# Kernel optimization log

Measured on AMD Instinct MI355X. Metric: run time of the kernel, lower is better.

Reference implementation:

```python
import jax, jax.numpy as jnp
import numpy as np

B, T, H = 2, 1024, 4096
HK, HV, DK, DV = 8, 32, 64, 64
VPK = HV // HK            # value heads per key head = 4
KEY_DIM = HK * DK         # 512
VAL_DIM = HV * DV         # 2048
CONV_DIM = 2 * KEY_DIM + VAL_DIM  # 3072
KSZ = 4
EPS = 1e-5
L2_EPS = 1e-6


def _l2norm(x):
    return x * jax.lax.rsqrt(jnp.sum(x * x, axis=-1, keepdims=True) + L2_EPS)


def setup_inputs() -> dict:
    key = jax.random.key(0)
    ks = jax.random.split(key, 8)
    s = 0.02
    return {
        "hidden_states": jax.random.normal(ks[0], (B, T, H), jnp.float32),
        "W_qkvz": jax.random.normal(ks[1], (H, 2 * KEY_DIM + 2 * VAL_DIM), jnp.float32) * s,
        "W_ba": jax.random.normal(ks[2], (H, 2 * HV), jnp.float32) * s,
        "conv_w": jax.random.normal(ks[3], (CONV_DIM, KSZ), jnp.float32) * 0.1,
        "dt_bias": jnp.ones((HV,), jnp.float32),
        "A_log": jnp.log(jax.random.uniform(ks[4], (HV,), jnp.float32, 1.0, 16.0)),
        "norm_w": jnp.ones((DV,), jnp.float32),
        "W_out": jax.random.normal(ks[5], (VAL_DIM, H), jnp.float32) * s,
    }


def _forward(hidden_states, W_qkvz, W_ba, conv_w, dt_bias, A_log, norm_w, W_out):
    # --- projections ---
    qkvz = hidden_states @ W_qkvz                       # [B,T,5120]
    ba = hidden_states @ W_ba                           # [B,T,64]
    # fix_query_key_value_ordering: per key head [q(Dk), k(Dk), v(vpk*Dv), z(vpk*Dv)]
    qkvz = qkvz.reshape(B, T, HK, 2 * DK + 2 * VPK * DV)
    q = qkvz[..., :DK]                                  # [B,T,HK,DK]
    k = qkvz[..., DK:2 * DK]
    v = qkvz[..., 2 * DK:2 * DK + VPK * DV].reshape(B, T, HV, DV)
    z = qkvz[..., 2 * DK + VPK * DV:].reshape(B, T, HV, DV)
    ba = ba.reshape(B, T, HK, 2 * VPK)
    b = ba[..., :VPK].reshape(B, T, HV)
    a = ba[..., VPK:].reshape(B, T, HV)

    # --- causal depthwise conv over concatenated qkv, then silu ---
    mixed = jnp.concatenate(
        [q.reshape(B, T, KEY_DIM), k.reshape(B, T, KEY_DIM), v.reshape(B, T, VAL_DIM)], axis=-1)
    padded = jnp.pad(mixed, ((0, 0), (KSZ - 1, 0), (0, 0)))
    conv = sum(padded[:, j:j + T, :] * conv_w[:, j] for j in range(KSZ))
    conv = jax.nn.silu(conv)
    q = conv[..., :KEY_DIM].reshape(B, T, HK, DK)
    k = conv[..., KEY_DIM:2 * KEY_DIM].reshape(B, T, HK, DK)
    v = conv[..., 2 * KEY_DIM:].reshape(B, T, HV, DV)

    # --- fused GDN gating: g = -exp(A_log)*softplus(a+dt_bias), beta = sigmoid(b) ---
    g = -jnp.exp(A_log) * jax.nn.softplus(a + dt_bias)  # [B,T,HV]
    beta = jax.nn.sigmoid(b)                            # [B,T,HV]

    # --- q/k l2 norm + scale, broadcast key heads to value heads ---
    q = _l2norm(q) * (DK ** -0.5)
    k = _l2norm(k)
    q = jnp.repeat(q, VPK, axis=2)                      # [B,T,HV,DK]
    k = jnp.repeat(k, VPK, axis=2)

    # --- gated delta-rule recurrence over time ---
    def step(S, inp):
        qt, kt, vt, gt, bt = inp                        # qt/kt [B,HV,DK], vt [B,HV,DV]
        S = S * jnp.exp(gt)[..., None, None]            # decay
        pred = jnp.einsum('bhk,bhkv->bhv', kt, S)
        delta = (vt - pred) * bt[..., None]
        S = S + jnp.einsum('bhk,bhv->bhkv', kt, delta)
        o = jnp.einsum('bhk,bhkv->bhv', qt, S)
        return S, o

    xs = (q.transpose(1, 0, 2, 3), k.transpose(1, 0, 2, 3), v.transpose(1, 0, 2, 3),
          g.transpose(1, 0, 2), beta.transpose(1, 0, 2))
    S0 = jnp.zeros((B, HV, DK, DV), q.dtype)
    _, o = jax.lax.scan(step, S0, xs)                   # [T,B,HV,DV]
    o = o.transpose(1, 0, 2, 3)                         # [B,T,HV,DV]

    # --- gated RMSNorm (norm before gate) + out projection ---
    o_n = o * jax.lax.rsqrt(jnp.mean(o * o, axis=-1, keepdims=True) + EPS) * norm_w
    o_n = o_n * jax.nn.silu(z)
    return o_n.reshape(B, T, VAL_DIM) @ W_out           # [B,T,H]


def reference(hidden_states, W_qkvz, W_ba, conv_w, dt_bias, A_log, norm_w, W_out):
    return _forward(hidden_states, W_qkvz, W_ba, conv_w, dt_bias, A_log, norm_w, W_out)
```

## Files before the change

### kernel.cpp

```cpp
#include <hip/hip_runtime.h>
#include <hip/hip_bf16.h>
#include <cstdint>
#include <cstddef>


typedef __attribute__((ext_vector_type(8))) short short8;
typedef __attribute__((ext_vector_type(4))) float f32x4;

__device__ __forceinline__ short f2bf(float f) {
  union { float f; unsigned u; } x; x.f = f;
  unsigned r = x.u + 0x7fffu + ((x.u >> 16) & 1u);
  return (short)(r >> 16);
}

__device__ __forceinline__ void gl_lds16(const short* g, short* l) {
  __builtin_amdgcn_global_load_lds(
      (const __attribute__((address_space(1))) void*)g,
      (__attribute__((address_space(3))) void*)l, 16, 0, 0);
}

__global__ __launch_bounds__(256) void to_bf16_kernel(const float* __restrict__ x,
                                                      short* __restrict__ y) {
  int i = blockIdx.x * 256 + threadIdx.x;
  float4 v = ((const float4*)x)[i];
  ushort4 r;
  r.x = (unsigned short)f2bf(v.x);
  r.y = (unsigned short)f2bf(v.y);
  r.z = (unsigned short)f2bf(v.z);
  r.w = (unsigned short)f2bf(v.w);
  ((ushort4*)y)[i] = r;
}

__global__ __launch_bounds__(256) void transpose_w1(const float* __restrict__ Wq,
                                                    const float* __restrict__ Wba,
                                                    short* __restrict__ Wt) {
  __shared__ float tile[32][33];
  int n0 = blockIdx.x * 32;
  int k0 = blockIdx.y * 32;
  int t = threadIdx.x;
  int r = t >> 5;
  int c = t & 31;
#pragma unroll
  for (int i = 0; i < 4; ++i) {
    int kl = r + i * 8;
    int n = n0 + c;
    float v = 0.f;
    if (n < 5120) v = Wq[(size_t)(k0 + kl) * 5120 + n];
    else if (n < 5184) v = Wba[(size_t)(k0 + kl) * 64 + (n - 5120)];
    tile[kl][c] = v;
  }
  __syncthreads();
#pragma unroll
  for (int i = 0; i < 4; ++i) {
    int nl = r + i * 8;
    int kl = c;
    Wt[(size_t)(n0 + nl) * 4096 + k0 + kl] = f2bf(tile[kl][nl]);
  }
}

__global__ __launch_bounds__(256) void transpose_w2(const float* __restrict__ W,
                                                    short* __restrict__ Wt) {
  __shared__ float tile[32][33];
  int n0 = blockIdx.x * 32;
  int k0 = blockIdx.y * 32;
  int t = threadIdx.x;
  int r = t >> 5;
  int c = t & 31;
#pragma unroll
  for (int i = 0; i < 4; ++i) {
    int kl = r + i * 8;
    tile[kl][c] = W[(size_t)(k0 + kl) * 4096 + n0 + c];
  }
  __syncthreads();
#pragma unroll
  for (int i = 0; i < 4; ++i) {
    int nl = r + i * 8;
    int kl = c;
    Wt[(size_t)(n0 + nl) * 2048 + k0 + kl] = f2bf(tile[kl][nl]);
  }
}

template <bool GUARD_N>
__global__ __launch_bounds__(128) void gemm128w2(const short* __restrict__ A,
                                                 const short* __restrict__ Bt,
                                                 float* __restrict__ C,
                                                 int N, int K, int MT) {
  __shared__ __align__(16) short As[3 * 4096];
  __shared__ __align__(16) short Bs[3 * 4096];
  const int tid = threadIdx.x;
  const int w = tid >> 6, lane = tid & 63;

  const int nwg = gridDim.x;
  const int bid = blockIdx.x;
  const int swz = (bid & 7) * (nwg >> 3) + (bid >> 3);
  const int m0 = (swz % MT) * 128;
  const int n0 = (swz / MT) * 128;

  const int rp0 = tid >> 3, q0 = tid & 7;
  const int mm0 = q0 ^ (rp0 & 7);
  const int srow = rp0 * 2 + (mm0 >> 2);
  const int scol = (mm0 & 3) << 3;
  const short* Ag = A + (size_t)(m0 + srow) * K + scol;
  const short* Bg = Bt + (size_t)(n0 + srow) * K + scol;
  const size_t rstep = (size_t)32 * K;

  const int fr = lane & 15;
  const int s = lane >> 4;
  int aoff[4], boff[8];
#pragma unroll
  for (int i = 0; i < 4; ++i) {
    int row = w * 64 + i * 16 + fr;
    int rp = row >> 1;
    int q = (((row & 1) << 2) | s) ^ (rp & 7);
    aoff[i] = (rp * 8 + q) * 8;
  }
#pragma unroll
  for (int j = 0; j < 8; ++j) {
    int row = j * 16 + fr;
    int rp = row >> 1;
    int q = (((row & 1) << 2) | s) ^ (rp & 7);
    boff[j] = (rp * 8 + q) * 8;
  }

  f32x4 acc[4][8];
#pragma unroll
  for (int i = 0; i < 4; ++i)
#pragma unroll
    for (int j = 0; j < 8; ++j) acc[i][j] = (f32x4){0.f, 0.f, 0.f, 0.f};

  const int NKT = K >> 5;

#define STAGE_A(kt, bb)                                                  \
  { const short* g = Ag + (size_t)(kt) * 32;                             \
    gl_lds16(g,             &As[(bb) * 4096 + (w << 9)]);                \
    gl_lds16(g + rstep,     &As[(bb) * 4096 + 1024 + (w << 9)]);         \
    gl_lds16(g + 2 * rstep, &As[(bb) * 4096 + 2048 + (w << 9)]);         \
    gl_lds16(g + 3 * rstep, &As[(bb) * 4096 + 3072 + (w << 9)]); }
#define STAGE_B(kt, bb)                                                  \
  { const short* g = Bg + (size_t)(kt) * 32;                             \
    gl_lds16(g,             &Bs[(bb) * 4096 + (w << 9)]);                \
    gl_lds16(g + rstep,     &Bs[(bb) * 4096 + 1024 + (w << 9)]);         \
    gl_lds16(g + 2 * rstep, &Bs[(bb) * 4096 + 2048 + (w << 9)]);         \
    gl_lds16(g + 3 * rstep, &Bs[(bb) * 4096 + 3072 + (w << 9)]); }

  STAGE_A(0, 0); STAGE_B(0, 0);
  STAGE_A(1, 1); STAGE_B(1, 1);
  asm volatile("s_waitcnt vmcnt(8)" ::: "memory");
  __builtin_amdgcn_s_barrier();
  __builtin_amdgcn_sched_barrier(0);

  int bi = 0;
  for (int kt = 0; kt < NKT; ++kt) {
    int bi2 = bi - 1; if (bi2 < 0) bi2 = 2;
    const short* Ab = &As[bi * 4096];
    const short* Bb = &Bs[bi * 4096];
    short8 af[4], bf[4];
#pragma unroll
    for (int i = 0; i < 4; ++i) af[i] = *(const short8*)&Ab[aoff[i]];
#pragma unroll
    for (int j = 0; j < 4; ++j) bf[j] = *(const short8*)&Bb[boff[j]];
    if (kt + 2 < NKT) STAGE_A(kt + 2, bi2);
    __builtin_amdgcn_s_barrier();
    asm volatile("s_waitcnt lgkmcnt(0)" ::: "memory");
    __builtin_amdgcn_sched_barrier(0);
    __builtin_amdgcn_s_setprio(1);
#pragma unroll
    for (int i = 0; i < 4; ++i)
#pragma unroll
      for (int j = 0; j < 4; ++j)
        acc[i][j] = __builtin_amdgcn_mfma_f32_16x16x32_bf16(af[i], bf[j], acc[i][j], 0, 0, 0);
    __builtin_amdgcn_s_setprio(0);
    __builtin_amdgcn_sched_barrier(0);
#pragma unroll
    for (int j = 0; j < 4; ++j) bf[j] = *(const short8*)&Bb[boff[j + 4]];
    if (kt + 2 < NKT) STAGE_B(kt + 2, bi2);
    if (kt < NKT - 2) { asm volatile("s_waitcnt vmcnt(8)" ::: "memory"); }
    else              { asm volatile("s_waitcnt vmcnt(0)" ::: "memory"); }
    __builtin_amdgcn_s_barrier();
    asm volatile("s_waitcnt lgkmcnt(0)" ::: "memory");
    __builtin_amdgcn_sched_barrier(0);
    __builtin_amdgcn_s_setprio(1);
#pragma unroll
    for (int i = 0; i < 4; ++i)
#pragma unroll
      for (int j = 0; j < 4; ++j)
        acc[i][j + 4] = __builtin_amdgcn_mfma_f32_16x16x32_bf16(af[i], bf[j], acc[i][j + 4], 0, 0, 0);
    __builtin_amdgcn_s_setprio(0);
    __builtin_amdgcn_sched_barrier(0);
    __builtin_amdgcn_s_barrier();
    ++bi; if (bi == 3) bi = 0;
  }
#undef STAGE_A
#undef STAGE_B

  const int rbase = (lane >> 4) << 2;
#pragma unroll
  for (int i = 0; i < 4; ++i) {
#pragma unroll
    for (int j = 0; j < 8; ++j) {
      int col = n0 + j * 16 + fr;
      if (GUARD_N && col >= N) continue;
      int row = m0 + w * 64 + i * 16 + rbase;
#pragma unroll
      for (int r = 0; r < 4; ++r)
        C[(size_t)(row + r) * N + col] = acc[i][j][r];
    }
  }
}

__global__ __launch_bounds__(256) void conv_kernel(const float* __restrict__ qkvz,
                                                   const float* __restrict__ conv_w,
                                                   float* __restrict__ mix) {
  __shared__ float sq[1024];
  __shared__ float scale[16];
  int bt = blockIdx.x;
  int t = bt & 1023;
  int tid = threadIdx.x;
  for (int c = tid; c < 3072; c += 256) {
    int col;
    if (c < 512) {
      col = (c >> 6) * 640 + (c & 63);
    } else if (c < 1024) {
      int c2 = c - 512;
      col = (c2 >> 6) * 640 + 64 + (c2 & 63);
    } else {
      int c3 = c - 1024;
      int hv = c3 >> 6;
      col = (hv >> 2) * 640 + 128 + (hv & 3) * 64 + (c3 & 63);
    }
    float acc = 0.f;
#pragma unroll
    for (int j = 0; j < 4; ++j) {
      int tt = t - 3 + j;
      if (tt >= 0) acc += qkvz[(size_t)(bt - 3 + j) * 5184 + col] * conv_w[c * 4 + j];
    }
    float sv = acc / (1.f + __expf(-acc));
    if (c < 1024)
      sq[c] = sv;
    else
      mix[(size_t)bt * 3072 + c] = sv;
  }
  __syncthreads();
  int g = tid >> 4, l = tid & 15;
  float p = 0.f;
#pragma unroll
  for (int i = 0; i < 4; ++i) {
    float v = sq[g * 64 + l * 4 + i];
    p += v * v;
  }
  p += __shfl_xor(p, 1);
  p += __shfl_xor(p, 2);
  p += __shfl_xor(p, 4);
  p += __shfl_xor(p, 8);
  if (l == 0) scale[g] = rsqrtf(p + 1e-6f);
  __syncthreads();
  for (int c = tid; c < 1024; c += 256) {
    float s = scale[c >> 6] * ((c < 512) ? 0.125f : 1.f);
    mix[(size_t)bt * 3072 + c] = sq[c] * s;
  }
}

__global__ __launch_bounds__(256) void gate_kernel(const float* __restrict__ qkvz,
                                                   const float* __restrict__ dt_bias,
                                                   const float* __restrict__ A_log,
                                                   float* __restrict__ gb,
                                                   float* __restrict__ beta) {
  int i = blockIdx.x * 256 + threadIdx.x;
  int hv = i & 31;
  int bt = i >> 5;
  int hk = hv >> 2, vp = hv & 3;
  const float* row = qkvz + (size_t)bt * 5184 + 5120 + hk * 8;
  float bv = row[vp];
  float av = row[4 + vp];
  float x = av + dt_bias[hv];
  float sp = (x > 20.f) ? x : log1pf(expf(x));
  gb[i] = -expf(A_log[hv]) * sp;
  beta[i] = 1.f / (1.f + expf(-bv));
}

__global__ __launch_bounds__(256) void precompute_kernel(
    const float* __restrict__ mix, const float* __restrict__ gbuf,
    const float* __restrict__ betab, float* __restrict__ Wbuf,
    float* __restrict__ Pbuf, float* __restrict__ Rbuf, float* __restrict__ cbuf) {
  __shared__ float Kt[64][68];
  __shared__ float Vb[64][68];
  __shared__ float AM[64][68];
  __shared__ float Mm[64][68];
  __shared__ float Tb[16][17];
  __shared__ float cs[64], bb[64];

  const int u = blockIdx.x;
  const int chunk = u & 15, hv = (u >> 4) & 31, b = u >> 9;
  const int hk = hv >> 2;
  const int t0g = b * 1024 + chunk * 64;
  const int tid = threadIdx.x;
  const int tr = tid >> 2, q4 = tid & 3;

  {
    const float* mrow = mix + (size_t)(t0g + tr) * 3072;
#pragma unroll
    for (int e = 0; e < 4; ++e) {
      int c0 = q4 * 16 + e * 4;
      float4 kv = *(const float4*)(mrow + 512 + hk * 64 + c0);
      Kt[c0 + 0][tr] = kv.x; Kt[c0 + 1][tr] = kv.y;
      Kt[c0 + 2][tr] = kv.z; Kt[c0 + 3][tr] = kv.w;
      *(float4*)&Vb[tr][c0] = *(const float4*)(mrow + 1024 + hv * 64 + c0);
    }
  }
  if (tid < 64) {
    cs[tid] = gbuf[(size_t)(t0g + tid) * 32 + hv];
    bb[tid] = betab[(size_t)(t0g + tid) * 32 + hv];
  }
  __syncthreads();
  for (int off = 1; off < 64; off <<= 1) {
    float v = 0.f;
    if (tid < 64 && tid >= off) v = cs[tid - off];
    __syncthreads();
    if (tid < 64) cs[tid] += v;
    __syncthreads();
  }
  if (tid < 64) cbuf[(size_t)u * 64 + tid] = cs[tid];

  {
    float acc[16];
#pragma unroll
    for (int i = 0; i < 16; ++i) acc[i] = 0.f;
    for (int d = 0; d < 64; ++d) {
      float kv = Kt[d][tr];
#pragma unroll
      for (int e = 0; e < 4; ++e) {
        float4 ks = *(const float4*)&Kt[d][q4 * 16 + e * 4];
        acc[e * 4 + 0] += kv * ks.x; acc[e * 4 + 1] += kv * ks.y;
        acc[e * 4 + 2] += kv * ks.z; acc[e * 4 + 3] += kv * ks.w;
      }
    }
    float bt_ = bb[tr], ct_ = cs[tr];
#pragma unroll
    for (int j = 0; j < 16; ++j) {
      int s = q4 * 16 + j;
      AM[tr][s] = (s < tr) ? bt_ * acc[j] * __expf(ct_ - cs[s]) : 0.f;
    }
  }
  __syncthreads();

  for (int i = tid; i < 64 * 68; i += 256) (&Mm[0][0])[i] = 0.f;
  __syncthreads();
  if (tid < 64) {
    int blk = tid >> 4, j = tid & 15, base = blk * 16;
    Mm[base][base + j] = (j == 0) ? 1.f : 0.f;
    for (int r = 1; r < 16; ++r) {
      float sum = 0.f;
      for (int s = 0; s < r; ++s) sum += AM[base + r][base + s] * Mm[base + s][base + j];
      Mm[base + r][base + j] = ((r == j) ? 1.f : 0.f) - sum;
    }
  }
  __syncthreads();
  for (int d = 1; d < 4; ++d) {
    for (int j = 0; j + d < 4; ++j) {
      int i = j + d;
      int r = tid >> 4, c = tid & 15;
      float tsum = 0.f;
      for (int kb = j; kb < i; ++kb)
        for (int uu = 0; uu < 16; ++uu)
          tsum += AM[i * 16 + r][kb * 16 + uu] * Mm[kb * 16 + uu][j * 16 + c];
      Tb[r][c] = tsum;
      __syncthreads();
      float msum = 0.f;
      for (int uu = 0; uu < 16; ++uu)
        msum += Mm[i * 16 + r][i * 16 + uu] * Tb[uu][c];
      __syncthreads();
      Mm[i * 16 + r][j * 16 + c] = -msum;
      __syncthreads();
    }
  }

  {
    const float* mrow = mix + (size_t)(t0g + tr) * 3072 + hk * 64;
#pragma unroll
    for (int e = 0; e < 4; ++e) {
      int c0 = q4 * 16 + e * 4;
      float4 qv = *(const float4*)(mrow + c0);
      AM[c0 + 0][tr] = qv.x; AM[c0 + 1][tr] = qv.y;
      AM[c0 + 2][tr] = qv.z; AM[c0 + 3][tr] = qv.w;
    }
  }
  __syncthreads();

  {
    float acc[16];
#pragma unroll
    for (int i = 0; i < 16; ++i) acc[i] = 0.f;
    for (int d = 0; d < 64; ++d) {
      float qv = AM[d][tr];
#pragma unroll
      for (int e = 0; e < 4; ++e) {
        float4 ks = *(const float4*)&Kt[d][q4 * 16 + e * 4];
        acc[e * 4 + 0] += qv * ks.x; acc[e * 4 + 1] += qv * ks.y;
        acc[e * 4 + 2] += qv * ks.z; acc[e * 4 + 3] += qv * ks.w;
      }
    }
    float ct_ = cs[tr];
#pragma unroll
    for (int e = 0; e < 4; ++e) {
      int s0 = q4 * 16 + e * 4;
      float4 pv;
      pv.x = (s0 + 0 <= tr) ? acc[e * 4 + 0] * __expf(ct_ - cs[s0 + 0]) : 0.f;
      pv.y = (s0 + 1 <= tr) ? acc[e * 4 + 1] * __expf(ct_ - cs[s0 + 1]) : 0.f;
      pv.z = (s0 + 2 <= tr) ? acc[e * 4 + 2] * __expf(ct_ - cs[s0 + 2]) : 0.f;
      pv.w = (s0 + 3 <= tr) ? acc[e * 4 + 3] * __expf(ct_ - cs[s0 + 3]) : 0.f;
      *(float4*)&Pbuf[(size_t)u * 4096 + tr * 64 + s0] = pv;
    }
  }
  __syncthreads();

  {
    float vals[16];
#pragma unroll
    for (int j = 0; j < 16; ++j) vals[j] = Kt[q4 * 16 + j][tr];
    float sc = bb[tr] * __expf(cs[tr]);
    __syncthreads();
#pragma unroll
    for (int j = 0; j < 16; ++j) Kt[tr][q4 * 16 + j] = vals[j] * sc;
  }
  __syncthreads();

  {
    float acc[16];
#pragma unroll
    for (int i = 0; i < 16; ++i) acc[i] = 0.f;
    for (int s = 0; s < 64; ++s) {
      float m = Mm[tr][s];
#pragma unroll
      for (int e = 0; e < 4; ++e) {
        float4 kk = *(const float4*)&Kt[s][q4 * 16 + e * 4];
        acc[e * 4 + 0] += m * kk.x; acc[e * 4 + 1] += m * kk.y;
        acc[e * 4 + 2] += m * kk.z; acc[e * 4 + 3] += m * kk.w;
      }
    }
#pragma unroll
    for (int e = 0; e < 4; ++e) {
      float4 wv = {acc[e * 4 + 0], acc[e * 4 + 1], acc[e * 4 + 2], acc[e * 4 + 3]};
      *(float4*)&Wbuf[(size_t)u * 4096 + tr * 64 + q4 * 16 + e * 4] = wv;
    }
  }
  {
    float acc[16];
#pragma unroll
    for (int i = 0; i < 16; ++i) acc[i] = 0.f;
    for (int s = 0; s < 64; ++s) {
      float m = Mm[tr][s] * bb[s];
#pragma unroll
      for (int e = 0; e < 4; ++e) {
        float4 vv = *(const float4*)&Vb[s][q4 * 16 + e * 4];
        acc[e * 4 + 0] += m * vv.x; acc[e * 4 + 1] += m * vv.y;
        acc[e * 4 + 2] += m * vv.z; acc[e * 4 + 3] += m * vv.w;
      }
    }
#pragma unroll
    for (int e = 0; e < 4; ++e) {
      float4 rv = {acc[e * 4 + 0], acc[e * 4 + 1], acc[e * 4 + 2], acc[e * 4 + 3]};
      *(float4*)&Rbuf[(size_t)u * 4096 + tr * 64 + q4 * 16 + e * 4] = rv;
    }
  }
}

__global__ __launch_bounds__(256) void precompute2_kernel(
    const float* __restrict__ mix, const float* __restrict__ cbuf,
    float* __restrict__ Wbuf, float* __restrict__ Pbuf, float* __restrict__ Rbuf,
    float* __restrict__ Hbuf) {
  __shared__ float At[64][132];
  __shared__ float Bsm[64][188];

  const int u = blockIdx.x;
  const int chunk = u & 15, hv = (u >> 4) & 31, b = u >> 9;
  const int hk = hv >> 2;
  const int t0g = b * 1024 + chunk * 64;
  const int tid = threadIdx.x;
  const int tr = tid >> 2, q4 = tid & 3;

  const float c63 = cbuf[(size_t)u * 64 + 63];
  const float csr = cbuf[(size_t)u * 64 + tr];
  const float sKv = __expf(c63 - csr);

  {
    const float* Pr = Pbuf + (size_t)u * 4096 + tr * 64;
#pragma unroll
    for (int e = 0; e < 4; ++e) {
      int k0 = q4 * 16 + e * 4;
      float4 p4 = *(const float4*)(Pr + k0);
      At[k0 + 0][tr] = p4.x; At[k0 + 1][tr] = p4.y;
      At[k0 + 2][tr] = p4.z; At[k0 + 3][tr] = p4.w;
    }
    const float* Kr = mix + (size_t)(t0g + tr) * 3072 + 512 + hk * 64;
#pragma unroll
    for (int e = 0; e < 4; ++e) {
      int n = q4 * 16 + e * 4;
      float4 k4 = *(const float4*)(Kr + n);
      float4 o4 = {k4.x * sKv, k4.y * sKv, k4.z * sKv, k4.w * sKv};
      *(float4*)&At[tr][64 + n] = o4;
    }
  }
  {
    const float* Wr = Wbuf + (size_t)u * 4096 + tr * 64;
    const float* Rr = Rbuf + (size_t)u * 4096 + tr * 64;
#pragma unroll
    for (int e = 0; e < 4; ++e) {
      int n = q4 * 16 + e * 4;
      int cp = n + ((n >> 3) << 2);
      *(float4*)&Bsm[tr][cp] = *(const float4*)(Wr + n);
      *(float4*)&Bsm[tr][cp + 96] = *(const float4*)(Rr + n);
    }
  }
  __syncthreads();

  const int m0 = (tid >> 4) << 3;
  const int n0 = (tid & 15) << 3;
  const int cb = n0 + ((n0 >> 3) << 2);
  float acc[8][8];
#pragma unroll
  for (int i = 0; i < 8; ++i)
#pragma unroll
    for (int j = 0; j < 8; ++j) acc[i][j] = 0.f;

  for (int k = 0; k < 64; ++k) {
    float4 a0 = *(const float4*)&At[k][m0];
    float4 a1 = *(const float4*)&At[k][m0 + 4];
    float4 b0 = *(const float4*)&Bsm[k][cb];
    float4 b1 = *(const float4*)&Bsm[k][cb + 4];
    float am[8] = {a0.x, a0.y, a0.z, a0.w, a1.x, a1.y, a1.z, a1.w};
    float bn[8] = {b0.x, b0.y, b0.z, b0.w, b1.x, b1.y, b1.z, b1.w};
#pragma unroll
    for (int i = 0; i < 8; ++i)
#pragma unroll
      for (int j = 0; j < 8; ++j) acc[i][j] += am[i] * bn[j];
  }

  if (m0 < 64) {
    if (n0 < 64) {
#pragma unroll
      for (int i = 0; i < 8; ++i) {
        int t = m0 + i;
        float ee = __expf(cbuf[(size_t)u * 64 + t]);
        const float* Qr = mix + (size_t)(t0g + t) * 3072 + hk * 64 + n0;
        float4 q0 = *(const float4*)(Qr);
        float4 q1 = *(const float4*)(Qr + 4);
        float4 g0 = {q0.x * ee - acc[i][0], q0.y * ee - acc[i][1],
                     q0.z * ee - acc[i][2], q0.w * ee - acc[i][3]};
        float4 g1 = {q1.x * ee - acc[i][4], q1.y * ee - acc[i][5],
                     q1.z * ee - acc[i][6], q1.w * ee - acc[i][7]};
        float* dst = Wbuf + (size_t)u * 4096 + t * 64 + n0;
        *(float4*)dst = g0; *(float4*)(dst + 4) = g1;
      }
    } else {
#pragma unroll
      for (int i = 0; i < 8; ++i) {
        float* dst = Rbuf + (size_t)u * 4096 + (m0 + i) * 64 + (n0 - 64);
        float4 r0 = {acc[i][0], acc[i][1], acc[i][2], acc[i][3]};
        float4 r1 = {acc[i][4], acc[i][5], acc[i][6], acc[i][7]};
        *(float4*)dst = r0; *(float4*)(dst + 4) = r1;
      }
    }
  } else {
    if (n0 < 64) {
#pragma unroll
      for (int i = 0; i < 8; ++i) {
        float* dst = Hbuf + (size_t)u * 4096 + (m0 - 64 + i) * 64 + n0;
        float4 h0 = {acc[i][0], acc[i][1], acc[i][2], acc[i][3]};
        float4 h1 = {acc[i][4], acc[i][5], acc[i][6], acc[i][7]};
        *(float4*)dst = h0; *(float4*)(dst + 4) = h1;
      }
    } else {
#pragma unroll
      for (int i = 0; i < 8; ++i) {
        float* dst = Pbuf + (size_t)u * 4096 + (m0 - 64 + i) * 64 + (n0 - 64);
        float4 k0v = {acc[i][0], acc[i][1], acc[i][2], acc[i][3]};
        float4 k1v = {acc[i][4], acc[i][5], acc[i][6], acc[i][7]};
        *(float4*)dst = k0v; *(float4*)(dst + 4) = k1v;
      }
    }
  }
}

__global__ __launch_bounds__(512) void chunk_scan_kernel(
    const float* __restrict__ Gbuf, const float* __restrict__ Hbuf,
    const float* __restrict__ ORbuf, const float* __restrict__ KRbuf,
    const float* __restrict__ cbuf, float* __restrict__ o) {
  __shared__ float Gs[64][68], Hs[64][68];
  __shared__ float St[16][68];

  const int bid = blockIdx.x;
  const int vs = bid & 3, hv = (bid >> 2) & 31, b = bid >> 7;
  const int bh = b * 32 + hv;
  const int ubase = bh * 16;
  const int tid = threadIdx.x;
  const int tr = tid >> 3, q8 = tid & 7;
  const int c0 = q8 * 2, c1 = q8 * 2 + 1;

  for (int i = tid; i < 16 * 68; i += 512) (&St[0][0])[i] = 0.f;

  float4 GN[2], HN[2];
  float2 ORn, KRn;
  float e63n = 0.f;

#define ISSUE(ch)                                                               \
  {                                                                             \
    size_t uu = (size_t)(ubase + (ch));                                         \
    _Pragma("unroll") for (int i = 0; i < 2; ++i) {                             \
      GN[i] = ((const float4*)(Gbuf + uu * 4096))[tid + 512 * i];               \
      HN[i] = ((const float4*)(Hbuf + uu * 4096))[tid + 512 * i];               \
    }                                                                           \
    ORn = *(const float2*)(ORbuf + uu * 4096 + tr * 64 + vs * 16 + q8 * 2);     \
    KRn = *(const float2*)(KRbuf + uu * 4096 + tr * 64 + vs * 16 + q8 * 2);     \
    e63n = cbuf[uu * 64 + 63];                                                  \
  }

#define COMMIT()                                                                \
  {                                                                             \
    _Pragma("unroll") for (int i = 0; i < 2; ++i) {                             \
      int flat = (tid + 512 * i) * 4;                                           \
      int rr = flat >> 6, cc = flat & 63;                                       \
      *(float4*)&Gs[rr][cc] = GN[i];                                            \
      *(float4*)&Hs[rr][cc] = HN[i];                                            \
    }                                                                           \
  }

  ISSUE(0);
  COMMIT();
  float2 ORv = ORn, KRv = KRn;
  float e63 = __expf(e63n);
  __syncthreads();

  for (int c = 0; c < 16; ++c) {
    if (c < 15) ISSUE(c + 1);
    float op0 = ORv.x, op1 = ORv.y, sn0 = KRv.x, sn1 = KRv.y;
    float sold0 = St[c0][tr], sold1 = St[c1][tr];
#pragma unroll
    for (int i = 0; i < 16; ++i) {
      float4 g4 = *(const float4*)&Gs[tr][i * 4];
      float4 h4 = *(const float4*)&Hs[tr][i * 4];
      float4 sa = *(const float4*)&St[c0][i * 4];
      float4 sb = *(const float4*)&St[c1][i * 4];
      op0 += g4.x * sa.x + g4.y * sa.y + g4.z * sa.z + g4.w * sa.w;
      op1 += g4.x * sb.x + g4.y * sb.y + g4.z * sb.z + g4.w * sb.w;
      sn0 -= h4.x * sa.x + h4.y * sa.y + h4.z * sa.z + h4.w * sa.w;
      sn1 -= h4.x * sb.x + h4.y * sb.y + h4.z * sb.z + h4.w * sb.w;
    }
    *(float2*)&o[((size_t)(bh * 4 + vs) * 1024 + c * 64 + tr) * 16 + q8 * 2] =
        (float2){op0, op1};
    float snew0 = sold0 * e63 + sn0;
    float snew1 = sold1 * e63 + sn1;
    __syncthreads();
    St[c0][tr] = snew0;
    St[c1][tr] = snew1;
    if (c < 15) {
      COMMIT();
      ORv = ORn; KRv = KRn; e63 = __expf(e63n);
    }
    __syncthreads();
  }
#undef ISSUE
#undef COMMIT
}

__global__ __launch_bounds__(256) void rms_gate_kernel(const float* __restrict__ o,
                                                       const float* __restrict__ qkvz,
                                                       const float* __restrict__ norm_w,
                                                       short* __restrict__ on) {
  int bid = blockIdx.x;
  int bh = bid >> 8;
  int tg = bid & 255;
  int b = bh >> 5, hv = bh & 31;
  int t = tg * 4 + (threadIdx.x >> 6);
  int d = threadIdx.x & 63;
  int bt = b * 1024 + t;
  int hk = hv >> 2, vp = hv & 3;
  float x = o[((size_t)(bh * 4 + (d >> 4)) * 1024 + t) * 16 + (d & 15)];
  float ss = x * x;
  ss += __shfl_xor(ss, 1);
  ss += __shfl_xor(ss, 2);
  ss += __shfl_xor(ss, 4);
  ss += __shfl_xor(ss, 8);
  ss += __shfl_xor(ss, 16);
  ss += __shfl_xor(ss, 32);
  float sc = rsqrtf(ss * (1.f / 64.f) + 1e-5f);
  float z = qkvz[(size_t)bt * 5184 + hk * 640 + 384 + vp * 64 + d];
  float val = x * sc * norm_w[d] * (z / (1.f + __expf(-z)));
  on[((size_t)bt * 32 + hv) * 64 + d] = f2bf(val);
}

extern "C" void kernel_launch(void* const* d_in, const int* in_sizes, int n_in,
                              void* d_out, int out_size, void* d_ws, size_t ws_size,
                              hipStream_t stream) {
  const float* hidden = (const float*)d_in[0];
  const float* W_qkvz = (const float*)d_in[1];
  const float* W_ba = (const float*)d_in[2];
  const float* conv_w = (const float*)d_in[3];
  const float* dt_bias = (const float*)d_in[4];
  const float* A_log = (const float*)d_in[5];
  const float* norm_w = (const float*)d_in[6];
  const float* W_out = (const float*)d_in[7];
  float* out = (float*)d_out;

  char* ws = (char*)d_ws;
  short* A_bf = (short*)(ws + 0);
  float* Hbuf = (float*)(ws + 0);
  short* Wt1 = (short*)(ws + 16777216);
  short* Wt2 = (short*)(ws + 59768832);
  float* qkvz = (float*)(ws + 76546048);
  float* mix = (float*)(ws + 119013376);
  float* gbuf = (float*)(ws + 144179200);
  float* beta = (float*)(ws + 144441344);
  float* o = (float*)(ws + 144703488);
  short* on = (short*)(ws + 161480704);
  float* Wbuf = (float*)(ws + 169869312);
  float* Pbuf = (float*)(ws + 186646528);
  float* Rbuf = (float*)(ws + 203423744);
  float* cbuf = (float*)(ws + 220200960);

  to_bf16_kernel<<<8192, 256, 0, stream>>>(hidden, A_bf);
  transpose_w1<<<dim3(164, 128), 256, 0, stream>>>(W_qkvz, W_ba, Wt1);
  transpose_w2<<<dim3(128, 64), 256, 0, stream>>>(W_out, Wt2);
  gemm128w2<true><<<656, 128, 0, stream>>>(A_bf, Wt1, qkvz, 5184, 4096, 16);
  conv_kernel<<<2048, 256, 0, stream>>>(qkvz, conv_w, mix);
  gate_kernel<<<256, 256, 0, stream>>>(qkvz, dt_bias, A_log, gbuf, beta);
  precompute_kernel<<<1024, 256, 0, stream>>>(mix, gbuf, beta, Wbuf, Pbuf, Rbuf, cbuf);
  precompute2_kernel<<<1024, 256, 0, stream>>>(mix, cbuf, Wbuf, Pbuf, Rbuf, Hbuf);
  chunk_scan_kernel<<<256, 512, 0, stream>>>(Wbuf, Hbuf, Rbuf, Pbuf, cbuf, o);
  rms_gate_kernel<<<16384, 256, 0, stream>>>(o, qkvz, norm_w, on);
  gemm128w2<false><<<512, 128, 0, stream>>>(on, Wt2, out, 4096, 2048, 16);
}
```

Measured before the change: 556.9 us.

## Use 4-wave GEMM, fuse gate into conv, register-tile precompute matmuls

The bf16 GEMM now runs 256 threads in a 2x2 wave grid, each wave computing a 64x64 sub-tile instead of 64x128, which lowers per-wave accumulator registers and adds waves per block. The separate gate kernel is folded into the conv kernel, saving one launch. The small 64x64 matmuls in precompute_kernel are rewritten with 4x4 register blocking, and the W and R products are fused into one loop so Mm is read only once. The change raises occupancy and reuse, at the cost of more barrier participants per block and different LDS access patterns.

Measured after the change: 536.0 us. 1.04x faster.

```diff
diff --git a/kernel.cpp b/kernel.cpp
--- a/kernel.cpp
+++ b/kernel.cpp
@@ -81,14 +81,15 @@
 }
 
 template <bool GUARD_N>
-__global__ __launch_bounds__(128) void gemm128w2(const short* __restrict__ A,
-                                                 const short* __restrict__ Bt,
-                                                 float* __restrict__ C,
-                                                 int N, int K, int MT) {
+__global__ __launch_bounds__(256) void gemm128p(const short* __restrict__ A,
+                                                const short* __restrict__ Bt,
+                                                float* __restrict__ C,
+                                                int N, int K, int MT) {
   __shared__ __align__(16) short As[3 * 4096];
   __shared__ __align__(16) short Bs[3 * 4096];
   const int tid = threadIdx.x;
   const int w = tid >> 6, lane = tid & 63;
+  const int wm = w >> 1, wn = w & 1;
 
   const int nwg = gridDim.x;
   const int bid = blockIdx.x;
@@ -96,56 +97,53 @@
   const int m0 = (swz % MT) * 128;
   const int n0 = (swz / MT) * 128;
 
-  const int rp0 = tid >> 3, q0 = tid & 7;
+  const int p0 = w * 64 + lane;
+  const int rp0 = p0 >> 3, q0 = p0 & 7;
   const int mm0 = q0 ^ (rp0 & 7);
   const int srow = rp0 * 2 + (mm0 >> 2);
   const int scol = (mm0 & 3) << 3;
   const short* Ag = A + (size_t)(m0 + srow) * K + scol;
   const short* Bg = Bt + (size_t)(n0 + srow) * K + scol;
-  const size_t rstep = (size_t)32 * K;
+  const size_t rstep = (size_t)64 * K;
 
   const int fr = lane & 15;
   const int s = lane >> 4;
-  int aoff[4], boff[8];
+  int aoff[4], boff[4];
 #pragma unroll
   for (int i = 0; i < 4; ++i) {
-    int row = w * 64 + i * 16 + fr;
+    int row = wm * 64 + i * 16 + fr;
     int rp = row >> 1;
     int q = (((row & 1) << 2) | s) ^ (rp & 7);
     aoff[i] = (rp * 8 + q) * 8;
   }
 #pragma unroll
-  for (int j = 0; j < 8; ++j) {
-    int row = j * 16 + fr;
+  for (int j = 0; j < 4; ++j) {
+    int row = wn * 64 + j * 16 + fr;
     int rp = row >> 1;
     int q = (((row & 1) << 2) | s) ^ (rp & 7);
     boff[j] = (rp * 8 + q) * 8;
   }
 
-  f32x4 acc[4][8];
+  f32x4 acc[4][4];
 #pragma unroll
   for (int i = 0; i < 4; ++i)
 #pragma unroll
-    for (int j = 0; j < 8; ++j) acc[i][j] = (f32x4){0.f, 0.f, 0.f, 0.f};
+    for (int j = 0; j < 4; ++j) acc[i][j] = (f32x4){0.f, 0.f, 0.f, 0.f};
 
   const int NKT = K >> 5;
 
-#define STAGE_A(kt, bb)                                                  \
-  { const short* g = Ag + (size_t)(kt) * 32;                             \
-    gl_lds16(g,             &As[(bb) * 4096 + (w << 9)]);                \
-    gl_lds16(g + rstep,     &As[(bb) * 4096 + 1024 + (w << 9)]);         \
-    gl_lds16(g + 2 * rstep, &As[(bb) * 4096 + 2048 + (w << 9)]);         \
-    gl_lds16(g + 3 * rstep, &As[(bb) * 4096 + 3072 + (w << 9)]); }
-#define STAGE_B(kt, bb)                                                  \
-  { const short* g = Bg + (size_t)(kt) * 32;                             \
-    gl_lds16(g,             &Bs[(bb) * 4096 + (w << 9)]);                \
-    gl_lds16(g + rstep,     &Bs[(bb) * 4096 + 1024 + (w << 9)]);         \
-    gl_lds16(g + 2 * rstep, &Bs[(bb) * 4096 + 2048 + (w << 9)]);         \
-    gl_lds16(g + 3 * rstep, &Bs[(bb) * 4096 + 3072 + (w << 9)]); }
+#define STAGE_A(kt, bb)                                                \
+  { const short* g = Ag + (size_t)(kt) * 32;                           \
+    gl_lds16(g,         &As[(bb) * 4096 + w * 512]);                   \
+    gl_lds16(g + rstep, &As[(bb) * 4096 + 2048 + w * 512]); }
+#define STAGE_B(kt, bb)                                                \
+  { const short* g = Bg + (size_t)(kt) * 32;                           \
+    gl_lds16(g,         &Bs[(bb) * 4096 + w * 512]);                   \
+    gl_lds16(g + rstep, &Bs[(bb) * 4096 + 2048 + w * 512]); }
 
   STAGE_A(0, 0); STAGE_B(0, 0);
   STAGE_A(1, 1); STAGE_B(1, 1);
-  asm volatile("s_waitcnt vmcnt(8)" ::: "memory");
+  asm volatile("s_waitcnt vmcnt(4)" ::: "memory");
   __builtin_amdgcn_s_barrier();
   __builtin_amdgcn_sched_barrier(0);
 
@@ -154,9 +152,9 @@
     int bi2 = bi - 1; if (bi2 < 0) bi2 = 2;
     const short* Ab = &As[bi * 4096];
     const short* Bb = &Bs[bi * 4096];
-    short8 af[4], bf[4];
-#pragma unroll
-    for (int i = 0; i < 4; ++i) af[i] = *(const short8*)&Ab[aoff[i]];
+    short8 af[2], bf[4];
+#pragma unroll
+    for (int i = 0; i < 2; ++i) af[i] = *(const short8*)&Ab[aoff[i]];
 #pragma unroll
     for (int j = 0; j < 4; ++j) bf[j] = *(const short8*)&Bb[boff[j]];
     if (kt + 2 < NKT) STAGE_A(kt + 2, bi2);
@@ -165,26 +163,26 @@
     __builtin_amdgcn_sched_barrier(0);
     __builtin_amdgcn_s_setprio(1);
 #pragma unroll
-    for (int i = 0; i < 4; ++i)
+    for (int i = 0; i < 2; ++i)
 #pragma unroll
       for (int j = 0; j < 4; ++j)
         acc[i][j] = __builtin_amdgcn_mfma_f32_16x16x32_bf16(af[i], bf[j], acc[i][j], 0, 0, 0);
     __builtin_amdgcn_s_setprio(0);
     __builtin_amdgcn_sched_barrier(0);
 #pragma unroll
-    for (int j = 0; j < 4; ++j) bf[j] = *(const short8*)&Bb[boff[j + 4]];
+    for (int i = 0; i < 2; ++i) af[i] = *(const short8*)&Ab[aoff[i + 2]];
     if (kt + 2 < NKT) STAGE_B(kt + 2, bi2);
-    if (kt < NKT - 2) { asm volatile("s_waitcnt vmcnt(8)" ::: "memory"); }
+    if (kt < NKT - 2) { asm volatile("s_waitcnt vmcnt(4)" ::: "memory"); }
     else              { asm volatile("s_waitcnt vmcnt(0)" ::: "memory"); }
     __builtin_amdgcn_s_barrier();
     asm volatile("s_waitcnt lgkmcnt(0)" ::: "memory");
     __builtin_amdgcn_sched_barrier(0);
     __builtin_amdgcn_s_setprio(1);
 #pragma unroll
-    for (int i = 0; i < 4; ++i)
+    for (int i = 0; i < 2; ++i)
 #pragma unroll
       for (int j = 0; j < 4; ++j)
-        acc[i][j + 4] = __builtin_amdgcn_mfma_f32_16x16x32_bf16(af[i], bf[j], acc[i][j + 4], 0, 0, 0);
+        acc[i + 2][j] = __builtin_amdgcn_mfma_f32_16x16x32_bf16(af[i], bf[j], acc[i + 2][j], 0, 0, 0);
     __builtin_amdgcn_s_setprio(0);
     __builtin_amdgcn_sched_barrier(0);
     __builtin_amdgcn_s_barrier();
@@ -197,10 +195,10 @@
 #pragma unroll
   for (int i = 0; i < 4; ++i) {
 #pragma unroll
-    for (int j = 0; j < 8; ++j) {
-      int col = n0 + j * 16 + fr;
+    for (int j = 0; j < 4; ++j) {
+      int col = n0 + wn * 64 + j * 16 + fr;
       if (GUARD_N && col >= N) continue;
-      int row = m0 + w * 64 + i * 16 + rbase;
+      int row = m0 + wm * 64 + i * 16 + rbase;
 #pragma unroll
       for (int r = 0; r < 4; ++r)
         C[(size_t)(row + r) * N + col] = acc[i][j][r];
@@ -210,7 +208,11 @@
 
 __global__ __launch_bounds__(256) void conv_kernel(const float* __restrict__ qkvz,
                                                    const float* __restrict__ conv_w,
-                                                   float* __restrict__ mix) {
+                                                   const float* __restrict__ dt_bias,
+                                                   const float* __restrict__ A_log,
+                                                   float* __restrict__ mix,
+                                                   float* __restrict__ gb,
+                                                   float* __restrict__ beta) {
   __shared__ float sq[1024];
   __shared__ float scale[16];
   int bt = blockIdx.x;
@@ -240,6 +242,17 @@
     else
       mix[(size_t)bt * 3072 + c] = sv;
   }
+  if (tid < 32) {
+    int hv2 = tid;
+    int hk2 = hv2 >> 2, vp = hv2 & 3;
+    const float* row = qkvz + (size_t)bt * 5184 + 5120 + hk2 * 8;
+    float bv = row[vp];
+    float av = row[4 + vp];
+    float x = av + dt_bias[hv2];
+    float sp = (x > 20.f) ? x : log1pf(expf(x));
+    gb[(size_t)bt * 32 + hv2] = -expf(A_log[hv2]) * sp;
+    beta[(size_t)bt * 32 + hv2] = 1.f / (1.f + expf(-bv));
+  }
   __syncthreads();
   int g = tid >> 4, l = tid & 15;
   float p = 0.f;
@@ -258,24 +271,6 @@
     float s = scale[c >> 6] * ((c < 512) ? 0.125f : 1.f);
     mix[(size_t)bt * 3072 + c] = sq[c] * s;
   }
-}
-
-__global__ __launch_bounds__(256) void gate_kernel(const float* __restrict__ qkvz,
-                                                   const float* __restrict__ dt_bias,
-                                                   const float* __restrict__ A_log,
-                                                   float* __restrict__ gb,
-                                                   float* __restrict__ beta) {
-  int i = blockIdx.x * 256 + threadIdx.x;
-  int hv = i & 31;
-  int bt = i >> 5;
-  int hk = hv >> 2, vp = hv & 3;
-  const float* row = qkvz + (size_t)bt * 5184 + 5120 + hk * 8;
-  float bv = row[vp];
-  float av = row[4 + vp];
-  float x = av + dt_bias[hv];
-  float sp = (x > 20.f) ? x : log1pf(expf(x));
-  gb[i] = -expf(A_log[hv]) * sp;
-  beta[i] = 1.f / (1.f + expf(-bv));
 }
 
 __global__ __launch_bounds__(256) void precompute_kernel(
@@ -295,6 +290,7 @@
   const int t0g = b * 1024 + chunk * 64;
   const int tid = threadIdx.x;
   const int tr = tid >> 2, q4 = tid & 3;
+  const int r4 = tid >> 4, c4 = tid & 15;
 
   {
     const float* mrow = mix + (size_t)(t0g + tr) * 3072;
@@ -322,23 +318,35 @@
   if (tid < 64) cbuf[(size_t)u * 64 + tid] = cs[tid];
 
   {
-    float acc[16];
-#pragma unroll
-    for (int i = 0; i < 16; ++i) acc[i] = 0.f;
+    float acc[4][4];
+#pragma unroll
+    for (int i = 0; i < 4; ++i)
+#pragma unroll
+      for (int j = 0; j < 4; ++j) acc[i][j] = 0.f;
     for (int d = 0; d < 64; ++d) {
-      float kv = Kt[d][tr];
-#pragma unroll
-      for (int e = 0; e < 4; ++e) {
-        float4 ks = *(const float4*)&Kt[d][q4 * 16 + e * 4];
-        acc[e * 4 + 0] += kv * ks.x; acc[e * 4 + 1] += kv * ks.y;
-        acc[e * 4 + 2] += kv * ks.z; acc[e * 4 + 3] += kv * ks.w;
+      float4 a4 = *(const float4*)&Kt[d][r4 * 4];
+      float4 b4 = *(const float4*)&Kt[d][c4 * 4];
+      float av[4] = {a4.x, a4.y, a4.z, a4.w};
+      float bv[4] = {b4.x, b4.y, b4.z, b4.w};
+#pragma unroll
+      for (int i = 0; i < 4; ++i)
+#pragma unroll
+        for (int j = 0; j < 4; ++j) acc[i][j] += av[i] * bv[j];
+    }
+    float4 cc = *(const float4*)&cs[c4 * 4];
+    float ccv[4] = {cc.x, cc.y, cc.z, cc.w};
+#pragma unroll
+    for (int i = 0; i < 4; ++i) {
+      int row = r4 * 4 + i;
+      float bt_ = bb[row], ct_ = cs[row];
+      float ov[4];
+#pragma unroll
+      for (int j = 0; j < 4; ++j) {
+        int sc = c4 * 4 + j;
+        ov[j] = (sc < row) ? bt_ * acc[i][j] * __expf(ct_ - ccv[j]) : 0.f;
       }
-    }
-    float bt_ = bb[tr], ct_ = cs[tr];
-#pragma unroll
-    for (int j = 0; j < 16; ++j) {
-      int s = q4 * 16 + j;
-      AM[tr][s] = (s < tr) ? bt_ * acc[j] * __expf(ct_ - cs[s]) : 0.f;
+      float4 o4 = {ov[0], ov[1], ov[2], ov[3]};
+      *(float4*)&AM[row][c4 * 4] = o4;
     }
   }
   __syncthreads();
@@ -387,28 +395,35 @@
   __syncthreads();
 
   {
-    float acc[16];
-#pragma unroll
-    for (int i = 0; i < 16; ++i) acc[i] = 0.f;
+    float acc[4][4];
+#pragma unroll
+    for (int i = 0; i < 4; ++i)
+#pragma unroll
+      for (int j = 0; j < 4; ++j) acc[i][j] = 0.f;
     for (int d = 0; d < 64; ++d) {
-      float qv = AM[d][tr];
-#pragma unroll
-      for (int e = 0; e < 4; ++e) {
-        float4 ks = *(const float4*)&Kt[d][q4 * 16 + e * 4];
-        acc[e * 4 + 0] += qv * ks.x; acc[e * 4 + 1] += qv * ks.y;
-        acc[e * 4 + 2] += qv * ks.z; acc[e * 4 + 3] += qv * ks.w;
+      float4 a4 = *(const float4*)&AM[d][r4 * 4];
+      float4 b4 = *(const float4*)&Kt[d][c4 * 4];
+      float av[4] = {a4.x, a4.y, a4.z, a4.w};
+      float bv[4] = {b4.x, b4.y, b4.z, b4.w};
+#pragma unroll
+      for (int i = 0; i < 4; ++i)
+#pragma unroll
+        for (int j = 0; j < 4; ++j) acc[i][j] += av[i] * bv[j];
+    }
+    float4 cc = *(const float4*)&cs[c4 * 4];
+    float ccv[4] = {cc.x, cc.y, cc.z, cc.w};
+#pragma unroll
+    for (int i = 0; i < 4; ++i) {
+      int row = r4 * 4 + i;
+      float ct_ = cs[row];
+      float pv[4];
+#pragma unroll
+      for (int j = 0; j < 4; ++j) {
+        int sc = c4 * 4 + j;
+        pv[j] = (sc <= row) ? acc[i][j] * __expf(ct_ - ccv[j]) : 0.f;
       }
-    }
-    float ct_ = cs[tr];
-#pragma unroll
-    for (int e = 0; e < 4; ++e) {
-      int s0 = q4 * 16 + e * 4;
-      float4 pv;
-      pv.x = (s0 + 0 <= tr) ? acc[e * 4 + 0] * __expf(ct_ - cs[s0 + 0]) : 0.f;
-      pv.y = (s0 + 1 <= tr) ? acc[e * 4 + 1] * __expf(ct_ - cs[s0 + 1]) : 0.f;
-      pv.z = (s0 + 2 <= tr) ? acc[e * 4 + 2] * __expf(ct_ - cs[s0 + 2]) : 0.f;
-      pv.w = (s0 + 3 <= tr) ? acc[e * 4 + 3] * __expf(ct_ - cs[s0 + 3]) : 0.f;
-      *(float4*)&Pbuf[(size_t)u * 4096 + tr * 64 + s0] = pv;
+      float4 p4 = {pv[0], pv[1], pv[2], pv[3]};
+      *(float4*)&Pbuf[(size_t)u * 4096 + row * 64 + c4 * 4] = p4;
     }
   }
   __syncthreads();
@@ -425,41 +440,47 @@
   __syncthreads();
 
   {
-    float acc[16];
-#pragma unroll
-    for (int i = 0; i < 16; ++i) acc[i] = 0.f;
-    for (int s = 0; s < 64; ++s) {
-      float m = Mm[tr][s];
-#pragma unroll
-      for (int e = 0; e < 4; ++e) {
-        float4 kk = *(const float4*)&Kt[s][q4 * 16 + e * 4];
-        acc[e * 4 + 0] += m * kk.x; acc[e * 4 + 1] += m * kk.y;
-        acc[e * 4 + 2] += m * kk.z; acc[e * 4 + 3] += m * kk.w;
+    float aw[4][4], ar[4][4];
+#pragma unroll
+    for (int i = 0; i < 4; ++i)
+#pragma unroll
+      for (int j = 0; j < 4; ++j) { aw[i][j] = 0.f; ar[i][j] = 0.f; }
+    for (int s0 = 0; s0 < 64; s0 += 4) {
+      float4 am[4];
+#pragma unroll
+      for (int i = 0; i < 4; ++i) am[i] = *(const float4*)&Mm[r4 * 4 + i][s0];
+      float4 bq = *(const float4*)&bb[s0];
+      float bbv[4] = {bq.x, bq.y, bq.z, bq.w};
+      float kv[4][4], vv[4][4];
+#pragma unroll
+      for (int uu = 0; uu < 4; ++uu) {
+        float4 k4 = *(const float4*)&Kt[s0 + uu][c4 * 4];
+        float4 v4 = *(const float4*)&Vb[s0 + uu][c4 * 4];
+        kv[uu][0] = k4.x; kv[uu][1] = k4.y; kv[uu][2] = k4.z; kv[uu][3] = k4.w;
+        vv[uu][0] = v4.x; vv[uu][1] = v4.y; vv[uu][2] = v4.z; vv[uu][3] = v4.w;
       }
-    }
-#pragma unroll
-    for (int e = 0; e < 4; ++e) {
-      float4 wv = {acc[e * 4 + 0], acc[e * 4 + 1], acc[e * 4 + 2], acc[e * 4 + 3]};
-      *(float4*)&Wbuf[(size_t)u * 4096 + tr * 64 + q4 * 16 + e * 4] = wv;
-    }
-  }
-  {
-    float acc[16];
-#pragma unroll
-    for (int i = 0; i < 16; ++i) acc[i] = 0.f;
-    for (int s = 0; s < 64; ++s) {
-      float m = Mm[tr][s] * bb[s];
-#pragma unroll
-      for (int e = 0; e < 4; ++e) {
-        float4 vv = *(const float4*)&Vb[s][q4 * 16 + e * 4];
-        acc[e * 4 + 0] += m * vv.x; acc[e * 4 + 1] += m * vv.y;
-        acc[e * 4 + 2] += m * vv.z; acc[e * 4 + 3] += m * vv.w;
+#pragma unroll
+      for (int i = 0; i < 4; ++i) {
+        float amv[4] = {am[i].x, am[i].y, am[i].z, am[i].w};
+#pragma unroll
+        for (int uu = 0; uu < 4; ++uu) {
+          float mw = amv[uu];
+          float mr = mw * bbv[uu];
+#pragma unroll
+          for (int j = 0; j < 4; ++j) {
+            aw[i][j] += mw * kv[uu][j];
+            ar[i][j] += mr * vv[uu][j];
+          }
+        }
       }
     }
 #pragma unroll
-    for (int e = 0; e < 4; ++e) {
-      float4 rv = {acc[e * 4 + 0], acc[e * 4 + 1], acc[e * 4 + 2], acc[e * 4 + 3]};
-      *(float4*)&Rbuf[(size_t)u * 4096 + tr * 64 + q4 * 16 + e * 4] = rv;
+    for (int i = 0; i < 4; ++i) {
+      int row = r4 * 4 + i;
+      float4 w4 = {aw[i][0], aw[i][1], aw[i][2], aw[i][3]};
+      float4 rr = {ar[i][0], ar[i][1], ar[i][2], ar[i][3]};
+      *(float4*)&Wbuf[(size_t)u * 4096 + row * 64 + c4 * 4] = w4;
+      *(float4*)&Rbuf[(size_t)u * 4096 + row * 64 + c4 * 4] = rr;
     }
   }
 }
@@ -720,12 +741,11 @@
   to_bf16_kernel<<<8192, 256, 0, stream>>>(hidden, A_bf);
   transpose_w1<<<dim3(164, 128), 256, 0, stream>>>(W_qkvz, W_ba, Wt1);
   transpose_w2<<<dim3(128, 64), 256, 0, stream>>>(W_out, Wt2);
-  gemm128w2<true><<<656, 128, 0, stream>>>(A_bf, Wt1, qkvz, 5184, 4096, 16);
-  conv_kernel<<<2048, 256, 0, stream>>>(qkvz, conv_w, mix);
-  gate_kernel<<<256, 256, 0, stream>>>(qkvz, dt_bias, A_log, gbuf, beta);
+  gemm128p<true><<<656, 256, 0, stream>>>(A_bf, Wt1, qkvz, 5184, 4096, 16);
+  conv_kernel<<<2048, 256, 0, stream>>>(qkvz, conv_w, dt_bias, A_log, mix, gbuf, beta);
   precompute_kernel<<<1024, 256, 0, stream>>>(mix, gbuf, beta, Wbuf, Pbuf, Rbuf, cbuf);
   precompute2_kernel<<<1024, 256, 0, stream>>>(mix, cbuf, Wbuf, Pbuf, Rbuf, Hbuf);
   chunk_scan_kernel<<<256, 512, 0, stream>>>(Wbuf, Hbuf, Rbuf, Pbuf, cbuf, o);
   rms_gate_kernel<<<16384, 256, 0, stream>>>(o, qkvz, norm_w, on);
-  gemm128w2<false><<<512, 128, 0, stream>>>(on, Wt2, out, 4096, 2048, 16);
-}
+  gemm128p<false><<<512, 256, 0, stream>>>(on, Wt2, out, 4096, 2048, 16);
+}
```
